# Optimization experiments

Hardware: AMD Instinct MI355X
Metric: run time of the kernel (lower is better)

The kernel has to match this reference:

```python
import jax, jax.numpy as jnp
import numpy as np

NEG_INF = -1e9
LRELU_SLOPE = 0.2

B, C, FIN, FOUT = 8, 2048, 128, 64


def setup_inputs() -> dict:
    key = jax.random.key(0)
    k1, k2, k3, k4 = jax.random.split(key, 4)
    H = jax.random.normal(k1, (B, C, FIN), dtype=jnp.float32)
    A = jax.random.randint(k2, (B, C, C), 0, 2, dtype=jnp.int32)
    W = jax.random.normal(k3, (FIN, FOUT), dtype=jnp.float32)
    a = jax.random.normal(k4, (2 * FOUT,), dtype=jnp.float32)
    return {"H": H, "A": A, "W": W, "a": a}


def reference(H, A, W, a):
    # Wh: [B, C, F]
    Wh = jnp.einsum("bcf,fo->bco", H, W)
    F = Wh.shape[-1]
    a1, a2 = a[:F], a[F:]
    # e_ij = a . concat(Wh_i, Wh_j) = (Wh_i . a1) + (Wh_j . a2)
    # -> never materialize the (B,C,C,2F) concat tensor; same math.
    s1 = jnp.einsum("bcf,f->bc", Wh, a1)  # [B, C] contribution of node i
    s2 = jnp.einsum("bcf,f->bc", Wh, a2)  # [B, C] contribution of node j
    e = jax.nn.leaky_relu(s1[:, :, None] + s2[:, None, :], LRELU_SLOPE)  # [B,C,C]
    mask = (A > 0) | jnp.eye(A.shape[-1], dtype=bool)[None]
    e = jnp.where(mask, e, NEG_INF)
    alpha = jax.nn.softmax(e, axis=-1)
    # dropout omitted (eval mode) for a deterministic correctness baseline
    out = jax.nn.relu(jnp.einsum("bij,bjf->bif", alpha, Wh))
    return out
```

## Files before the change

### kernel.cpp

```cpp
#include <hip/hip_runtime.h>

#define NB 8
#define NC 2048
#define KIN 128
#define NF 64

#define WTSTRIDE 136
#define RSTRIDE 68
#define MROW 264
#define MOFF 60.0f
#define LOG2E 1.44269504088896340736f

typedef float floatx4_t __attribute__((ext_vector_type(4)));
typedef __bf16 bf16x8_t __attribute__((ext_vector_type(8)));
typedef unsigned short ushort8_t __attribute__((ext_vector_type(8)));

static __device__ __forceinline__ unsigned short f2bf(float f) {
  union { float f; unsigned int u; } v; v.f = f;
  unsigned int u = v.u;
  u += 0x7FFFu + ((u >> 16) & 1u);
  return (unsigned short)(u >> 16);
}

static __device__ __forceinline__ float lrelu(float x) {
  return fmaxf(x, 0.2f * x);
}

__global__ __launch_bounds__(256, 4) void k1_prep(
    const float* __restrict__ H, const float* __restrict__ W,
    const float* __restrict__ avec,
    float* __restrict__ s1g, float* __restrict__ s2g,
    unsigned short* __restrict__ WhT)
{
  __shared__ unsigned short WTsh[NF * WTSTRIDE];
  __shared__ float w1sh[KIN];
  __shared__ float w2sh[KIN];

  const int t = threadIdx.x;
  const int b = blockIdx.x >> 7;
  const int c0 = (blockIdx.x & 127) * 16;

  for (int i = t; i < KIN * NF; i += 256) {
    int k = i >> 6, f = i & 63;
    WTsh[f * WTSTRIDE + k] = f2bf(W[i]);
  }
  if (t < KIN) {
    float acc1 = 0.f, acc2 = 0.f;
    const float* wr = W + t * NF;
#pragma unroll
    for (int f = 0; f < NF; ++f) {
      float wv = wr[f];
      acc1 += wv * avec[f];
      acc2 += wv * avec[NF + f];
    }
    w1sh[t] = acc1;
    w2sh[t] = acc2;
  }
  __syncthreads();

  {
    const int r = t >> 4;
    const int x = t & 15;
    const float* hp = H + (size_t)(b * NC + c0 + r) * KIN + x * 8;
    float4 h0 = *(const float4*)(hp);
    float4 h1 = *(const float4*)(hp + 4);
    float4 u10 = *(const float4*)(w1sh + x * 8);
    float4 u11 = *(const float4*)(w1sh + x * 8 + 4);
    float4 u20 = *(const float4*)(w2sh + x * 8);
    float4 u21 = *(const float4*)(w2sh + x * 8 + 4);
    float p1 = h0.x * u10.x + h0.y * u10.y + h0.z * u10.z + h0.w * u10.w
             + h1.x * u11.x + h1.y * u11.y + h1.z * u11.z + h1.w * u11.w;
    float p2 = h0.x * u20.x + h0.y * u20.y + h0.z * u20.z + h0.w * u20.w
             + h1.x * u21.x + h1.y * u21.y + h1.z * u21.z + h1.w * u21.w;
#pragma unroll
    for (int off = 1; off < 16; off <<= 1) {
      p1 += __shfl_xor(p1, off);
      p2 += __shfl_xor(p2, off);
    }
    if (x == 0) {
      s1g[b * NC + c0 + r] = p1;
      s2g[b * NC + c0 + r] = p2;
    }
  }

  const int wave = t >> 6;
  const int lane = t & 63;
  const int m = lane & 15;
  const int q = lane >> 4;
  floatx4_t acc = (floatx4_t){0.f, 0.f, 0.f, 0.f};

  const float* hb = H + (size_t)(b * NC + c0 + m) * KIN;
#pragma unroll
  for (int kt = 0; kt < 4; ++kt) {
    const int kbase = kt * 32 + q * 8;
    float4 h0 = *(const float4*)(hb + kbase);
    float4 h1 = *(const float4*)(hb + kbase + 4);
    ushort8_t bu;
    bu[0] = f2bf(h0.x); bu[1] = f2bf(h0.y); bu[2] = f2bf(h0.z); bu[3] = f2bf(h0.w);
    bu[4] = f2bf(h1.x); bu[5] = f2bf(h1.y); bu[6] = f2bf(h1.z); bu[7] = f2bf(h1.w);
    bf16x8_t bf = __builtin_bit_cast(bf16x8_t, bu);
    ushort8_t au = *(const ushort8_t*)(WTsh + (wave * 16 + m) * WTSTRIDE + kbase);
    bf16x8_t af = __builtin_bit_cast(bf16x8_t, au);
    acc = __builtin_amdgcn_mfma_f32_16x16x32_bf16(af, bf, acc, 0, 0, 0);
  }
#pragma unroll
  for (int i2 = 0; i2 < 4; ++i2) {
    const int f = wave * 16 + q * 4 + i2;
    WhT[(size_t)(b * NF + f) * NC + c0 + m] = f2bf(acc[i2]);
  }
}

__global__ __launch_bounds__(256, 4) void k2_attn(
    const int* __restrict__ A, const float* __restrict__ s1g,
    const float* __restrict__ s2g, const unsigned short* __restrict__ WhT,
    float* __restrict__ out)
{
  __shared__ float s2_sh[NC];
  __shared__ unsigned char mask_sh[16 * MROW];
  __shared__ float s1_sh[16];
  __shared__ float wmax_sh[4];
  __shared__ float red_sh[4 * 16 * RSTRIDE];
  __shared__ float lsum_sh[4 * 16];

  const int t = threadIdx.x;
  const int b = blockIdx.x >> 7;
  const int i0 = (blockIdx.x & 127) * 16;
  const int wave = t >> 6;
  const int lane = t & 63;

  float lmax;
  {
    const float* sp = s2g + b * NC;
    float4 v0 = *(const float4*)(sp + t * 4);
    float4 v1 = *(const float4*)(sp + 1024 + t * 4);
    *(float4*)(s2_sh + t * 4) = v0;
    *(float4*)(s2_sh + 1024 + t * 4) = v1;
    lmax = fmaxf(fmaxf(fmaxf(v0.x, v0.y), fmaxf(v0.z, v0.w)),
                 fmaxf(fmaxf(v1.x, v1.y), fmaxf(v1.z, v1.w)));
#pragma unroll
    for (int off = 1; off < 64; off <<= 1)
      lmax = fmaxf(lmax, __shfl_xor(lmax, off));
    if (lane == 0) wmax_sh[wave] = lmax;
  }
  if (t < 16) s1_sh[t] = s1g[b * NC + i0 + t];

#pragma unroll 2
  for (int rr = 0; rr < 4; ++rr) {
    const int row = wave * 4 + rr;
    const int gRow = i0 + row;
    const int* arow = A + ((size_t)b * NC + gRow) * NC;
#pragma unroll
    for (int span = 0; span < 4; ++span) {
      const int cbase = span * 512 + lane * 8;
      int4 a0 = *(const int4*)(arow + cbase);
      int4 a1 = *(const int4*)(arow + cbase + 4);
      unsigned int byte = 0;
      byte |= (a0.x > 0 || cbase + 0 == gRow) ? 1u : 0u;
      byte |= (a0.y > 0 || cbase + 1 == gRow) ? 2u : 0u;
      byte |= (a0.z > 0 || cbase + 2 == gRow) ? 4u : 0u;
      byte |= (a0.w > 0 || cbase + 3 == gRow) ? 8u : 0u;
      byte |= (a1.x > 0 || cbase + 4 == gRow) ? 16u : 0u;
      byte |= (a1.y > 0 || cbase + 5 == gRow) ? 32u : 0u;
      byte |= (a1.z > 0 || cbase + 6 == gRow) ? 64u : 0u;
      byte |= (a1.w > 0 || cbase + 7 == gRow) ? 128u : 0u;
      unsigned int v = byte;
      v |= ((unsigned int)__shfl_xor((int)v, 1)) << 8;
      v |= ((unsigned int)__shfl_xor((int)v, 2)) << 16;
      if ((lane & 3) == 0)
        *(unsigned int*)(mask_sh + row * MROW + span * 64 + lane) = v;
    }
  }
  __syncthreads();

  const float s2max =
      fmaxf(fmaxf(wmax_sh[0], wmax_sh[1]), fmaxf(wmax_sh[2], wmax_sh[3]));

  const int m = lane & 15;
  const int q = lane >> 4;
  const float s1m = s1_sh[m];
  const float mmL = (lrelu(s1m + s2max) - MOFF) * LOG2E;
  const unsigned short* whb = WhT + (size_t)b * NF * NC;

  ushort8_t ou;
  {
    const unsigned short ov = (m == 0) ? (unsigned short)0x3F80 : (unsigned short)0;
#pragma unroll
    for (int idx = 0; idx < 8; ++idx) ou[idx] = ov;
  }
  const bf16x8_t onesf = __builtin_bit_cast(bf16x8_t, ou);

  floatx4_t acc[4], accl;
#pragma unroll
  for (int nt = 0; nt < 4; ++nt) acc[nt] = (floatx4_t){0.f, 0.f, 0.f, 0.f};
  accl = (floatx4_t){0.f, 0.f, 0.f, 0.f};

  const int ktBeg = wave * 16;
  for (int kk = 0; kk < 16; ++kk) {
    const int kt = ktBeg + kk;
    const int jq = kt * 32 + q * 8;
    const unsigned int mb = mask_sh[m * MROW + kt * 4 + q];
    ushort8_t whc[4];
#pragma unroll
    for (int nt = 0; nt < 4; ++nt)
      whc[nt] = *(const ushort8_t*)(whb + (size_t)(nt * 16 + m) * NC + jq);

    float4 s0 = *(const float4*)(s2_sh + jq);
    float4 s1v = *(const float4*)(s2_sh + jq + 4);
    const float sv[8] = {s0.x, s0.y, s0.z, s0.w, s1v.x, s1v.y, s1v.z, s1v.w};
    uint4 pk;
#pragma unroll
    for (int pair = 0; pair < 4; ++pair) {
      float p0 = __builtin_amdgcn_exp2f(
          fmaf(lrelu(s1m + sv[2 * pair]), LOG2E, -mmL));
      float p1 = __builtin_amdgcn_exp2f(
          fmaf(lrelu(s1m + sv[2 * pair + 1]), LOG2E, -mmL));
      p0 = (mb & (1u << (2 * pair))) ? p0 : 0.0f;
      p1 = (mb & (2u << (2 * pair))) ? p1 : 0.0f;
      pk[pair] = __builtin_amdgcn_perm(__builtin_bit_cast(unsigned int, p1),
                                       __builtin_bit_cast(unsigned int, p0),
                                       0x07060302u);
    }
    const bf16x8_t af = __builtin_bit_cast(bf16x8_t, pk);
#pragma unroll
    for (int nt = 0; nt < 4; ++nt) {
      bf16x8_t bf = __builtin_bit_cast(bf16x8_t, whc[nt]);
      acc[nt] = __builtin_amdgcn_mfma_f32_16x16x32_bf16(af, bf, acc[nt], 0, 0, 0);
    }
    accl = __builtin_amdgcn_mfma_f32_16x16x32_bf16(af, onesf, accl, 0, 0, 0);
  }

#pragma unroll
  for (int nt = 0; nt < 4; ++nt) {
#pragma unroll
    for (int i2 = 0; i2 < 4; ++i2) {
      red_sh[wave * (16 * RSTRIDE) + (q * 4 + i2) * RSTRIDE + nt * 16 + m] =
          acc[nt][i2];
    }
  }
  if (m == 0) {
#pragma unroll
    for (int i2 = 0; i2 < 4; ++i2)
      lsum_sh[wave * 16 + q * 4 + i2] = accl[i2];
  }
  __syncthreads();

  {
    const int row = t >> 4;
    const int f0 = (t & 15) * 4;
    float4 v = {0.f, 0.f, 0.f, 0.f};
    float ls = 0.f;
#pragma unroll
    for (int w = 0; w < 4; ++w) {
      const float* rp = red_sh + w * (16 * RSTRIDE) + row * RSTRIDE + f0;
      float4 vv = *(const float4*)rp;
      v.x += vv.x; v.y += vv.y; v.z += vv.z; v.w += vv.w;
      ls += lsum_sh[w * 16 + row];
    }
    const float inv = 1.0f / ls;
    float4 o;
    o.x = fmaxf(v.x * inv, 0.f);
    o.y = fmaxf(v.y * inv, 0.f);
    o.z = fmaxf(v.z * inv, 0.f);
    o.w = fmaxf(v.w * inv, 0.f);
    *(float4*)(out + (size_t)(b * NC + i0 + row) * NF + f0) = o;
  }
}

extern "C" void kernel_launch(void* const* d_in, const int* in_sizes, int n_in,
                              void* d_out, int out_size, void* d_ws, size_t ws_size,
                              hipStream_t stream) {
  const float* H = (const float*)d_in[0];
  const int* A = (const int*)d_in[1];
  const float* W = (const float*)d_in[2];
  const float* avec = (const float*)d_in[3];
  float* out = (float*)d_out;

  char* ws = (char*)d_ws;
  unsigned short* WhT = (unsigned short*)ws;
  float* s1 = (float*)(ws + (size_t)NB * NF * NC * 2);
  float* s2 = s1 + NB * NC;

  k1_prep<<<dim3(NB * (NC / 16)), dim3(256), 0, stream>>>(H, W, avec, s1, s2, WhT);
  k2_attn<<<dim3(NB * (NC / 16)), dim3(256), 0, stream>>>(A, s1, s2, WhT, out);
}
```

Before: 239.7 us.

## Split adjacency bitmask packing into a separate pre-pass kernel

Adds a k0_mask kernel that reads the int32 adjacency matrix once, with one wave per row and all loads issued before use, and writes a packed 256-byte bitmask per row to workspace. k2_attn now loads its 16 rows of bitmask with one 16-byte load per thread instead of streaming and packing A itself. This moves the bandwidth-heavy A read (about 134 MB) out of the attention kernel, so that kernel can run without waiting on it. The cost is an extra launch and a small bitmask write and read, and the total A traffic stays the same.

Result: no change. 241.5 us (+0.7%).

```diff
diff --git a/kernel.cpp b/kernel.cpp
--- a/kernel.cpp
+++ b/kernel.cpp
@@ -7,7 +7,7 @@
 
 #define WTSTRIDE 136
 #define RSTRIDE 68
-#define MROW 264
+#define MROW 272
 #define MOFF 60.0f
 #define LOG2E 1.44269504088896340736f
 
@@ -24,6 +24,41 @@
 
 static __device__ __forceinline__ float lrelu(float x) {
   return fmaxf(x, 0.2f * x);
+}
+
+__global__ __launch_bounds__(256, 4) void k0_mask(
+    const int* __restrict__ A, unsigned char* __restrict__ maskG)
+{
+  const int wv = blockIdx.x * 4 + (threadIdx.x >> 6);
+  const int lane = threadIdx.x & 63;
+  const int r = wv & (NC - 1);
+  const int* arow = A + (size_t)wv * NC;
+
+  int4 v[8];
+#pragma unroll
+  for (int s = 0; s < 4; ++s) {
+    const int cbase = s * 512 + lane * 8;
+    v[2 * s]     = *(const int4*)(arow + cbase);
+    v[2 * s + 1] = *(const int4*)(arow + cbase + 4);
+  }
+
+  unsigned char* mrow = maskG + (size_t)wv * 256;
+#pragma unroll
+  for (int s = 0; s < 4; ++s) {
+    const int cbase = s * 512 + lane * 8;
+    const int4 a0 = v[2 * s];
+    const int4 a1 = v[2 * s + 1];
+    unsigned int byte = 0;
+    byte |= (a0.x > 0 || cbase + 0 == r) ? 1u : 0u;
+    byte |= (a0.y > 0 || cbase + 1 == r) ? 2u : 0u;
+    byte |= (a0.z > 0 || cbase + 2 == r) ? 4u : 0u;
+    byte |= (a0.w > 0 || cbase + 3 == r) ? 8u : 0u;
+    byte |= (a1.x > 0 || cbase + 4 == r) ? 16u : 0u;
+    byte |= (a1.y > 0 || cbase + 5 == r) ? 32u : 0u;
+    byte |= (a1.z > 0 || cbase + 6 == r) ? 64u : 0u;
+    byte |= (a1.w > 0 || cbase + 7 == r) ? 128u : 0u;
+    mrow[s * 64 + lane] = (unsigned char)byte;
+  }
 }
 
 __global__ __launch_bounds__(256, 4) void k1_prep(
@@ -111,7 +146,7 @@
 }
 
 __global__ __launch_bounds__(256, 4) void k2_attn(
-    const int* __restrict__ A, const float* __restrict__ s1g,
+    const unsigned char* __restrict__ maskG, const float* __restrict__ s1g,
     const float* __restrict__ s2g, const unsigned short* __restrict__ WhT,
     float* __restrict__ out)
 {
@@ -144,31 +179,12 @@
   }
   if (t < 16) s1_sh[t] = s1g[b * NC + i0 + t];
 
-#pragma unroll 2
-  for (int rr = 0; rr < 4; ++rr) {
-    const int row = wave * 4 + rr;
-    const int gRow = i0 + row;
-    const int* arow = A + ((size_t)b * NC + gRow) * NC;
-#pragma unroll
-    for (int span = 0; span < 4; ++span) {
-      const int cbase = span * 512 + lane * 8;
-      int4 a0 = *(const int4*)(arow + cbase);
-      int4 a1 = *(const int4*)(arow + cbase + 4);
-      unsigned int byte = 0;
-      byte |= (a0.x > 0 || cbase + 0 == gRow) ? 1u : 0u;
-      byte |= (a0.y > 0 || cbase + 1 == gRow) ? 2u : 0u;
-      byte |= (a0.z > 0 || cbase + 2 == gRow) ? 4u : 0u;
-      byte |= (a0.w > 0 || cbase + 3 == gRow) ? 8u : 0u;
-      byte |= (a1.x > 0 || cbase + 4 == gRow) ? 16u : 0u;
-      byte |= (a1.y > 0 || cbase + 5 == gRow) ? 32u : 0u;
-      byte |= (a1.z > 0 || cbase + 6 == gRow) ? 64u : 0u;
-      byte |= (a1.w > 0 || cbase + 7 == gRow) ? 128u : 0u;
-      unsigned int v = byte;
-      v |= ((unsigned int)__shfl_xor((int)v, 1)) << 8;
-      v |= ((unsigned int)__shfl_xor((int)v, 2)) << 16;
-      if ((lane & 3) == 0)
-        *(unsigned int*)(mask_sh + row * MROW + span * 64 + lane) = v;
-    }
+  {
+    const int row = t >> 4;
+    const int off = (t & 15) * 16;
+    const uint4 mv =
+        *(const uint4*)(maskG + (size_t)(b * NC + i0 + row) * 256 + off);
+    *(uint4*)(mask_sh + row * MROW + off) = mv;
   }
   __syncthreads();
 
@@ -279,7 +295,9 @@
   unsigned short* WhT = (unsigned short*)ws;
   float* s1 = (float*)(ws + (size_t)NB * NF * NC * 2);
   float* s2 = s1 + NB * NC;
-
+  unsigned char* maskG = (unsigned char*)(s2 + NB * NC);
+
+  k0_mask<<<dim3(NB * NC / 4), dim3(256), 0, stream>>>(A, maskG);
   k1_prep<<<dim3(NB * (NC / 16)), dim3(256), 0, stream>>>(H, W, avec, s1, s2, WhT);
-  k2_attn<<<dim3(NB * (NC / 16)), dim3(256), 0, stream>>>(A, s1, s2, WhT, out);
-}
+  k2_attn<<<dim3(NB * (NC / 16)), dim3(256), 0, stream>>>(maskG, s1, s2, WhT, out);
+}
```
